# Optimization experiments

Hardware: AMD Instinct MI355X
Metric: run time of the kernel (lower is better)

Reference implementation:

```python
import jax, jax.numpy as jnp
import numpy as np

N_NODES = 1048576
N_SEG = 16384
NODES_PER_SEG = N_NODES // N_SEG
D = 128
EPS = 1e-5


def setup_inputs() -> dict:
    key = jax.random.key(0)
    ks = jax.random.split(key, 8)
    feat = jax.random.normal(ks[0], (N_NODES, D), dtype=jnp.float32)
    position_weight = jax.random.uniform(ks[1], (N_NODES,), dtype=jnp.float32)
    # equal-size segments (sessions): contiguous, sorted segment ids
    segment_ids = jnp.repeat(jnp.arange(N_SEG, dtype=jnp.int32), NODES_PER_SEG)
    # last node of each segment
    last_nodes = jnp.arange(N_SEG, dtype=jnp.int32) * NODES_PER_SEG + (NODES_PER_SEG - 1)
    # parameters
    gamma = jnp.ones((D,), dtype=jnp.float32)
    beta = jnp.zeros((D,), dtype=jnp.float32)
    s = 1.0 / np.sqrt(D)
    W_u = jax.random.uniform(ks[2], (D, D), dtype=jnp.float32, minval=-s, maxval=s)
    W_i = jax.random.uniform(ks[3], (D, D), dtype=jnp.float32, minval=-s, maxval=s)
    b_i = jax.random.uniform(ks[4], (D,), dtype=jnp.float32, minval=-s, maxval=s)
    w_e = jax.random.uniform(ks[5], (D,), dtype=jnp.float32, minval=-s, maxval=s)
    return {
        "feat": feat, "position_weight": position_weight,
        "last_nodes": last_nodes, "segment_ids": segment_ids,
        "gamma": gamma, "beta": beta, "W_u": W_u, "W_i": W_i,
        "b_i": b_i, "w_e": w_e, "num_segments": N_SEG,
    }


def reference(feat, position_weight, last_nodes, segment_ids, gamma, beta,
              W_u, W_i, b_i, w_e, num_segments):
    # BatchNorm1d (training-mode batch statistics)
    mean = feat.mean(axis=0)
    var = jnp.mean((feat - mean) ** 2, axis=0)
    f = (feat - mean) * (gamma / jnp.sqrt(var + EPS)) + beta  # [N, D]

    feat_u = f @ W_u.T                                         # [N, H]
    feat_last = f[last_nodes] @ W_i.T + b_i                    # [B, H]
    # broadcast_nodes: gather per-graph vector back to its nodes
    e = jax.nn.sigmoid(feat_u + feat_last[segment_ids]) @ w_e  # [N]

    # segment softmax over nodes of each graph
    m = jax.ops.segment_max(e, segment_ids, num_segments=num_segments)
    ex = jnp.exp(e - m[segment_ids])
    denom = jax.ops.segment_sum(ex, segment_ids, num_segments=num_segments)
    alpha = ex / denom[segment_ids]                            # [N]

    rst = jax.ops.segment_sum(f * alpha[:, None], segment_ids,
                              num_segments=num_segments)       # [B, D]
    position_rst = jax.ops.segment_sum(f * position_weight[:, None], segment_ids,
                                       num_segments=num_segments)  # [B, D]
    return rst, position_rst
```

## Files before the change

### kernel.cpp

```cpp
#include <hip/hip_runtime.h>

#define N_NODES 1048576
#define N_SEG   16384
#define NPS     64
#define D       128
#define EPS     1e-5f

typedef float f4 __attribute__((ext_vector_type(4)));
typedef float f32x4 __attribute__((ext_vector_type(4)));
typedef __bf16 bf16x8 __attribute__((ext_vector_type(8)));
typedef unsigned u32x4 __attribute__((ext_vector_type(4)));

__global__ __launch_bounds__(256) void k_stats(const float* __restrict__ feat,
                                               float* __restrict__ part) {
    int t = threadIdx.x;
    long gid = (long)blockIdx.x * 256 + t;
    const f4* f4p = (const f4*)feat;
    f4 s = {0.f,0.f,0.f,0.f}, q = {0.f,0.f,0.f,0.f};
#pragma unroll 8
    for (int k = 0; k < 64; ++k) {
        f4 v = f4p[gid + (long)k * 524288];
        s += v;
        q += v * v;
    }
    __shared__ f4 red[2][8][32];
    red[0][t >> 5][t & 31] = s;
    red[1][t >> 5][t & 31] = q;
    __syncthreads();
    int stat = t >> 7, c = t & 127;
    const float* base = (const float*)&red[stat][0][0];
    float acc = 0.f;
#pragma unroll
    for (int r = 0; r < 8; ++r) acc += base[r * 128 + c];
    part[(stat * 128 + c) * 2048 + blockIdx.x] = acc;
}

__global__ __launch_bounds__(256) void k_scale(const float* __restrict__ part,
                                               const float* __restrict__ gamma,
                                               const float* __restrict__ beta,
                                               float* __restrict__ scl,
                                               float* __restrict__ shf) {
    int t = threadIdx.x, c = blockIdx.x;
    float s1 = 0.f, s2 = 0.f;
#pragma unroll
    for (int j = 0; j < 8; ++j) {
        s1 += part[c * 2048 + t + 256 * j];
        s2 += part[(128 + c) * 2048 + t + 256 * j];
    }
    __shared__ float rs[256], rq[256];
    rs[t] = s1; rq[t] = s2;
    __syncthreads();
    for (int off = 128; off > 0; off >>= 1) {
        if (t < off) { rs[t] += rs[t + off]; rq[t] += rq[t + off]; }
        __syncthreads();
    }
    if (t == 0) {
        float mean = rs[0] / (float)N_NODES;
        float var  = rq[0] / (float)N_NODES - mean * mean;
        float sc   = gamma[c] * rsqrtf(var + EPS);
        scl[c] = sc;
        shf[c] = beta[c] - mean * sc;
    }
}

__device__ inline unsigned pk2(float x, float y) {
    unsigned a = __builtin_bit_cast(unsigned, x);
    unsigned b = __builtin_bit_cast(unsigned, y);
    a = (a + 0x7fffu + ((a >> 16) & 1u)) >> 16;
    b = (b + 0x7fffu + ((b >> 16) & 1u)) & 0xffff0000u;
    return a | b;
}
__device__ inline bf16x8 lds8(const unsigned short* p, int row, int kb) {
    int addr = (row * 256 + kb) ^ ((row & 7) << 4);
    return *(const bf16x8*)((const char*)p + addr);
}
__device__ inline bf16x8 bfrag(const float* __restrict__ W, int h, int kk, int g4) {
    const float* p = W + h * 128 + kk * 32 + g4 * 8;
    f4 u = *(const f4*)p;
    f4 v = *(const f4*)(p + 4);
    u32x4 r = { pk2(u.x, u.y), pk2(u.z, u.w), pk2(v.x, v.y), pk2(v.z, v.w) };
    return __builtin_bit_cast(bf16x8, r);
}
__device__ inline void bar_lgkm() {
    __builtin_amdgcn_sched_barrier(0);
    asm volatile("s_waitcnt lgkmcnt(0)" ::: "memory");
    __builtin_amdgcn_s_barrier();
    __builtin_amdgcn_sched_barrier(0);
}

__global__ __launch_bounds__(256, 2) void k_main(const float* __restrict__ feat,
                                                 const float* __restrict__ pw,
                                                 const float* __restrict__ Wu,
                                                 const float* __restrict__ Wi,
                                                 const float* __restrict__ bi,
                                                 const float* __restrict__ we,
                                                 const float* __restrict__ scl,
                                                 const float* __restrict__ shf,
                                                 float* __restrict__ out) {
    __shared__ __align__(16) unsigned short abuf[64 * 128];
    __shared__ float flp_s[8][128];
    __shared__ float pw_s[512];
    __shared__ float epart[4][64];
    __shared__ float wpR[4][128];
    __shared__ float wpP[4][128];

    int t = threadIdx.x;
    int lane = t & 63, w = t >> 6;
    int l15 = lane & 15, g4 = lane >> 4;
    int c0 = 4 * (t & 31);
    f4 vscl = *(const f4*)(scl + c0);
    f4 vshf = *(const f4*)(shf + c0);
    int h_a = l15 + 32 * w;
    int h_b = h_a + 16;
    int seg0 = blockIdx.x * 8;

    f4 fnA[8], fnB[8];
    {
        const f4* srcA = (const f4*)(feat + (long)seg0 * NPS * D);
#pragma unroll
        for (int k = 0; k < 8; ++k) fnA[k] = srcA[t + 256 * k];
        const f4* srcB = (const f4*)(feat + (long)(seg0 + 1) * NPS * D);
#pragma unroll
        for (int k = 0; k < 8; ++k) fnB[k] = srcB[t + 256 * k];
    }
    __builtin_amdgcn_sched_barrier(0);

    pw_s[t] = pw[seg0 * NPS + t];
    pw_s[t + 256] = pw[seg0 * NPS + t + 256];
    {
        int r = t >> 5;
        long row = (long)(seg0 + r) * NPS + (NPS - 1);
        f4 v = *(const f4*)(feat + row * 128 + c0);
        v = v * vscl + vshf;
        int addr = (r * 256 + 8 * (t & 31)) ^ ((r & 7) << 4);
        *(uint2*)((char*)abuf + addr) = make_uint2(pk2(v.x, v.y), pk2(v.z, v.w));
        int r2 = r + 8;
        int addr2 = (r2 * 256 + 8 * (t & 31)) ^ ((r2 & 7) << 4);
        *(uint2*)((char*)abuf + addr2) = make_uint2(0u, 0u);
    }
    bar_lgkm();
    {
        f32x4 a2[2];
        a2[0] = (f32x4){0.f,0.f,0.f,0.f};
        a2[1] = (f32x4){0.f,0.f,0.f,0.f};
#pragma unroll
        for (int kk = 0; kk < 4; ++kk) {
            bf16x8 a = lds8(abuf, l15, kk * 64 + g4 * 16);
            a2[0] = __builtin_amdgcn_mfma_f32_16x16x32_bf16(a, bfrag(Wi, h_a, kk, g4), a2[0], 0, 0, 0);
            a2[1] = __builtin_amdgcn_mfma_f32_16x16x32_bf16(a, bfrag(Wi, h_b, kk, g4), a2[1], 0, 0, 0);
        }
        float bia = bi[h_a], bib = bi[h_b];
#pragma unroll
        for (int r = 0; r < 4; ++r) {
            int si = 4 * g4 + r;
            if (si < 8) {
                flp_s[si][h_a] = a2[0][r] + bia;
                flp_s[si][h_b] = a2[1][r] + bib;
            }
        }
    }
    bf16x8 bW[8];
#pragma unroll
    for (int kk = 0; kk < 4; ++kk) {
        bW[kk]     = bfrag(Wu, h_a, kk, g4);
        bW[4 + kk] = bfrag(Wu, h_b, kk, g4);
    }
    float we0 = we[h_a], we1 = we[h_b];
    bar_lgkm();

#define PROC_SEG(SL, FN, PSL)                                                        \
    do {                                                                             \
        int seg = seg0 + (SL);                                                       \
        _Pragma("unroll")                                                            \
        for (int k = 0; k < 8; ++k) {           \
            f4 v = FN[k] * vscl + vshf;                                              \
            int n = (t >> 5) + 8 * k;                                                \
            int addr = (n * 256 + 8 * (t & 31)) ^ ((n & 7) << 4);                    \
            *(uint2*)((char*)abuf + addr) = make_uint2(pk2(v.x, v.y), pk2(v.z, v.w));\
        }                                                                            \
        bar_lgkm();                               \
        if ((PSL) < 8) {                              \
            const f4* src = (const f4*)(feat + (long)(seg0 + (PSL)) * NPS * D);      \
            _Pragma("unroll")                                                        \
            for (int k = 0; k < 8; ++k) FN[k] = src[t + 256 * k];                    \
        }                                                                            \
        __builtin_amdgcn_sched_barrier(0);              \
        float fl0 = flp_s[(SL)][h_a];                                                \
        float fl1 = flp_s[(SL)][h_b];                                                \
        f32x4 acc[4][2];                                                             \
        _Pragma("unroll")                                                            \
        for (int nf = 0; nf < 4; ++nf) {                                             \
            acc[nf][0] = (f32x4){0.f,0.f,0.f,0.f};                                   \
            acc[nf][1] = (f32x4){0.f,0.f,0.f,0.f};                                   \
        }                                                                            \
        _Pragma("unroll")                                                            \
        for (int kk = 0; kk < 4; ++kk) {                                             \
            int kb = kk * 64 + g4 * 16;                                              \
            bf16x8 a[4];                                                             \
            _Pragma("unroll")                                                        \
            for (int nf = 0; nf < 4; ++nf) a[nf] = lds8(abuf, l15 + 16 * nf, kb);    \
            _Pragma("unroll")                                                        \
            for (int nf = 0; nf < 4; ++nf) {                                         \
                acc[nf][0] = __builtin_amdgcn_mfma_f32_16x16x32_bf16(a[nf], bW[kk],     acc[nf][0], 0, 0, 0); \
                acc[nf][1] = __builtin_amdgcn_mfma_f32_16x16x32_bf16(a[nf], bW[4 + kk], acc[nf][1], 0, 0, 0); \
            }                                                                        \
        }                                                                            \
        _Pragma("unroll")                                                            \
        for (int nf = 0; nf < 4; ++nf) {                                             \
            _Pragma("unroll")                                                        \
            for (int r = 0; r < 4; ++r) {                                            \
                float x0 = acc[nf][0][r] + fl0;                                      \
                float x1 = acc[nf][1][r] + fl1;                                      \
                float p = we0 / (1.f + __expf(-x0)) + we1 / (1.f + __expf(-x1));     \
                p += __shfl_xor(p, 1);                                               \
                p += __shfl_xor(p, 2);                                               \
                p += __shfl_xor(p, 4);                                               \
                p += __shfl_xor(p, 8);                                               \
                if (l15 == 0) epart[w][16 * nf + 4 * g4 + r] = p;                    \
            }                                                                        \
        }                                                                            \
        bar_lgkm();                                                 \
        float e = epart[0][lane] + epart[1][lane] + epart[2][lane] + epart[3][lane]; \
        float m = e;                                                                 \
        _Pragma("unroll")                                                            \
        for (int off = 32; off > 0; off >>= 1) m = fmaxf(m, __shfl_xor(m, off));     \
        float ex = __expf(e - m);                                                    \
        float sd = ex;                                                               \
        _Pragma("unroll")                                                            \
        for (int off = 32; off > 0; off >>= 1) sd += __shfl_xor(sd, off);            \
        float al = ex / sd;                                                          \
        f4 racc = {0.f,0.f,0.f,0.f}, pacc = {0.f,0.f,0.f,0.f};                       \
        _Pragma("unroll")                                                            \
        for (int k = 0; k < 8; ++k) {                                                \
            int n = (t >> 5) + 8 * k;                                                \
            int addr = (n * 256 + 8 * (t & 31)) ^ ((n & 7) << 4);                    \
            uint2 u = *(const uint2*)((const char*)abuf + addr);                     \
            f4 fv;                                                                   \
            fv.x = __builtin_bit_cast(float, u.x << 16);                             \
            fv.y = __builtin_bit_cast(float, u.x & 0xffff0000u);                     \
            fv.z = __builtin_bit_cast(float, u.y << 16);                             \
            fv.w = __builtin_bit_cast(float, u.y & 0xffff0000u);                     \
            float av = __shfl(al, n);                                                \
            float pv = pw_s[(SL) * NPS + n];                                         \
            racc += av * fv;                                                         \
            pacc += pv * fv;                                                         \
        }                                                                            \
        _Pragma("unroll")                                                            \
        for (int c = 0; c < 4; ++c) {                                                \
            racc[c] += __shfl_xor(racc[c], 32);                                      \
            pacc[c] += __shfl_xor(pacc[c], 32);                                      \
        }                                                                            \
        if (lane < 32) {                                                             \
            *(f4*)&wpR[w][4 * lane] = racc;                                          \
            *(f4*)&wpP[w][4 * lane] = pacc;                                          \
        }                                                                            \
        bar_lgkm();                                                    \
        if (t < 128) {                                                               \
            out[(long)seg * 128 + t] = wpR[0][t] + wpR[1][t] + wpR[2][t] + wpR[3][t];\
        } else {                                                                     \
            int c = t - 128;                                                         \
            out[(long)N_SEG * 128 + (long)seg * 128 + c] =                           \
                wpP[0][c] + wpP[1][c] + wpP[2][c] + wpP[3][c];                       \
        }                                                                            \
    } while (0)

    for (int it = 0; it < 8; it += 2) {
        PROC_SEG(it,     fnA, it + 2);
        PROC_SEG(it + 1, fnB, it + 3);
    }
#undef PROC_SEG
}

extern "C" void kernel_launch(void* const* d_in, const int* in_sizes, int n_in,
                              void* d_out, int out_size, void* d_ws, size_t ws_size,
                              hipStream_t stream) {
    const float* feat       = (const float*)d_in[0];
    const float* pw         = (const float*)d_in[1];
    const float* gamma      = (const float*)d_in[4];
    const float* beta       = (const float*)d_in[5];
    const float* Wu         = (const float*)d_in[6];
    const float* Wi         = (const float*)d_in[7];
    const float* bi         = (const float*)d_in[8];
    const float* we         = (const float*)d_in[9];
    float* out = (float*)d_out;

    float* ws   = (float*)d_ws;
    float* part = ws;
    float* wscl = ws + 524288;
    float* wshf = ws + 524288 + 128;

    k_stats<<<dim3(2048), dim3(256), 0, stream>>>(feat, part);
    k_scale<<<dim3(128),  dim3(256), 0, stream>>>(part, gamma, beta, wscl, wshf);
    k_main <<<dim3(2048), dim3(256), 0, stream>>>(feat, pw, Wu, Wi, bi, we, wscl, wshf, out);
}
```

Measured before the change: 353.0 us.

## Double-buffer segment output partials and keep normalized features in registers

```diff
diff --git a/kernel.cpp b/kernel.cpp
--- a/kernel.cpp
+++ b/kernel.cpp
@@ -81,9 +81,9 @@
     u32x4 r = { pk2(u.x, u.y), pk2(u.z, u.w), pk2(v.x, v.y), pk2(v.z, v.w) };
     return __builtin_bit_cast(bf16x8, r);
 }
-__device__ inline void bar_lgkm() {
+__device__ inline void barx() {
     __builtin_amdgcn_sched_barrier(0);
-    asm volatile("s_waitcnt lgkmcnt(0)" ::: "memory");
+    asm volatile("s_waitcnt lgkmcnt(0)");
     __builtin_amdgcn_s_barrier();
     __builtin_amdgcn_sched_barrier(0);
 }
@@ -101,8 +101,8 @@
     __shared__ float flp_s[8][128];
     __shared__ float pw_s[512];
     __shared__ float epart[4][64];
-    __shared__ float wpR[4][128];
-    __shared__ float wpP[4][128];
+    __shared__ float wpR[2][4][128];
+    __shared__ float wpP[2][4][128];
 
     int t = threadIdx.x;
     int lane = t & 63, w = t >> 6;
@@ -138,7 +138,7 @@
         int addr2 = (r2 * 256 + 8 * (t & 31)) ^ ((r2 & 7) << 4);
         *(uint2*)((char*)abuf + addr2) = make_uint2(0u, 0u);
     }
-    bar_lgkm();
+    barx();
     {
         f32x4 a2[2];
         a2[0] = (f32x4){0.f,0.f,0.f,0.f};
@@ -166,25 +166,37 @@
         bW[4 + kk] = bfrag(Wu, h_b, kk, g4);
     }
     float we0 = we[h_a], we1 = we[h_b];
-    bar_lgkm();
-
-#define PROC_SEG(SL, FN, PSL)                                                        \
+    barx();
+
+#define PROC_SEG(SL, FN, PSL, FIRST)                                                 \
     do {                                                                             \
         int seg = seg0 + (SL);                                                       \
+        f4 v[8];                                \
         _Pragma("unroll")                                                            \
         for (int k = 0; k < 8; ++k) {           \
-            f4 v = FN[k] * vscl + vshf;                                              \
+            v[k] = FN[k] * vscl + vshf;                                              \
             int n = (t >> 5) + 8 * k;                                                \
             int addr = (n * 256 + 8 * (t & 31)) ^ ((n & 7) << 4);                    \
-            *(uint2*)((char*)abuf + addr) = make_uint2(pk2(v.x, v.y), pk2(v.z, v.w));\
-        }                                                                            \
-        bar_lgkm();                               \
+            *(uint2*)((char*)abuf + addr) = make_uint2(pk2(v[k].x, v[k].y), pk2(v[k].z, v[k].w)); \
+        }                                                                            \
+        barx();                                                           \
         if ((PSL) < 8) {                              \
             const f4* src = (const f4*)(feat + (long)(seg0 + (PSL)) * NPS * D);      \
             _Pragma("unroll")                                                        \
             for (int k = 0; k < 8; ++k) FN[k] = src[t + 256 * k];                    \
         }                                                                            \
         __builtin_amdgcn_sched_barrier(0);              \
+        if (!(FIRST)) {                          \
+            int ps = seg - 1, pb = (SL + 1) & 1;                                     \
+            if (t < 128) {                                                           \
+                out[(long)ps * 128 + t] =                                            \
+                    wpR[pb][0][t] + wpR[pb][1][t] + wpR[pb][2][t] + wpR[pb][3][t];   \
+            } else {                                                                 \
+                int c = t - 128;                                                     \
+                out[(long)N_SEG * 128 + (long)ps * 128 + c] =                        \
+                    wpP[pb][0][c] + wpP[pb][1][c] + wpP[pb][2][c] + wpP[pb][3][c];   \
+            }                                                                        \
+        }                                                                            \
         float fl0 = flp_s[(SL)][h_a];                                                \
         float fl1 = flp_s[(SL)][h_b];                                                \
         f32x4 acc[4][2];                                                             \
@@ -219,7 +231,7 @@
                 if (l15 == 0) epart[w][16 * nf + 4 * g4 + r] = p;                    \
             }                                                                        \
         }                                                                            \
-        bar_lgkm();                                                 \
+        barx();                                                           \
         float e = epart[0][lane] + epart[1][lane] + epart[2][lane] + epart[3][lane]; \
         float m = e;                                                                 \
         _Pragma("unroll")                                                            \
@@ -231,19 +243,12 @@
         float al = ex / sd;                                                          \
         f4 racc = {0.f,0.f,0.f,0.f}, pacc = {0.f,0.f,0.f,0.f};                       \
         _Pragma("unroll")                                                            \
-        for (int k = 0; k < 8; ++k) {                                                \
+        for (int k = 0; k < 8; ++k) {         \
             int n = (t >> 5) + 8 * k;                                                \
-            int addr = (n * 256 + 8 * (t & 31)) ^ ((n & 7) << 4);                    \
-            uint2 u = *(const uint2*)((const char*)abuf + addr);                     \
-            f4 fv;                                                                   \
-            fv.x = __builtin_bit_cast(float, u.x << 16);                             \
-            fv.y = __builtin_bit_cast(float, u.x & 0xffff0000u);                     \
-            fv.z = __builtin_bit_cast(float, u.y << 16);                             \
-            fv.w = __builtin_bit_cast(float, u.y & 0xffff0000u);                     \
             float av = __shfl(al, n);                                                \
             float pv = pw_s[(SL) * NPS + n];                                         \
-            racc += av * fv;                                                         \
-            pacc += pv * fv;                                                         \
+            racc += av * v[k];                                                       \
+            pacc += pv * v[k];                                                       \
         }                                                                            \
         _Pragma("unroll")                                                            \
         for (int c = 0; c < 4; ++c) {                                                \
@@ -251,24 +256,26 @@
             pacc[c] += __shfl_xor(pacc[c], 32);                                      \
         }                                                                            \
         if (lane < 32) {                                                             \
-            *(f4*)&wpR[w][4 * lane] = racc;                                          \
-            *(f4*)&wpP[w][4 * lane] = pacc;                                          \
-        }                                                                            \
-        bar_lgkm();                                                    \
-        if (t < 128) {                                                               \
-            out[(long)seg * 128 + t] = wpR[0][t] + wpR[1][t] + wpR[2][t] + wpR[3][t];\
-        } else {                                                                     \
-            int c = t - 128;                                                         \
-            out[(long)N_SEG * 128 + (long)seg * 128 + c] =                           \
-                wpP[0][c] + wpP[1][c] + wpP[2][c] + wpP[3][c];                       \
+            *(f4*)&wpR[(SL) & 1][w][4 * lane] = racc;                                \
+            *(f4*)&wpP[(SL) & 1][w][4 * lane] = pacc;                                \
         }                                                                            \
     } while (0)
 
     for (int it = 0; it < 8; it += 2) {
-        PROC_SEG(it,     fnA, it + 2);
-        PROC_SEG(it + 1, fnB, it + 3);
+        PROC_SEG(it,     fnA, it + 2, it == 0);
+        PROC_SEG(it + 1, fnB, it + 3, false);
     }
 #undef PROC_SEG
+
+    barx();
+    if (t < 128) {
+        out[(long)(seg0 + 7) * 128 + t] =
+            wpR[1][0][t] + wpR[1][1][t] + wpR[1][2][t] + wpR[1][3][t];
+    } else {
+        int c = t - 128;
+        out[(long)N_SEG * 128 + (long)(seg0 + 7) * 128 + c] =
+            wpP[1][0][c] + wpP[1][1][c] + wpP[1][2][c] + wpP[1][3][c];
+    }
 }
 
 extern "C" void kernel_launch(void* const* d_in, const int* in_sizes, int n_in,
```

Measured after the change: 353.3 us. Within noise of the previous version (+0.1%).
